# Kernel tuning notes

Measured on AMD Instinct MI355X. Metric: run time of the kernel, lower is better.

Reference implementation:

```python
import jax, jax.numpy as jnp
import numpy as np

H = 4                      # attention heads
N_A, N_P = 20000, 30000    # author / paper node counts
E = 200000                 # edges per edge type
IN, HID, OUT = 256, 256, 128
NEG_SLOPE = 0.2


def setup_inputs() -> dict:
    key = jax.random.key(0)
    ks = jax.random.split(key, 24)

    def w(k, shape, fan_in):
        return jax.random.normal(k, shape, jnp.float32) / np.float32(np.sqrt(fan_in))

    inp = {
        'x_author': jax.random.normal(ks[0], (N_A, IN), jnp.float32),
        'x_paper':  jax.random.normal(ks[1], (N_P, IN), jnp.float32),
        'src_ap': jax.random.randint(ks[2], (E,), 0, N_A, jnp.int32),
        'dst_ap': jax.random.randint(ks[3], (E,), 0, N_P, jnp.int32),
        'src_pa': jax.random.randint(ks[4], (E,), 0, N_P, jnp.int32),
        'dst_pa': jax.random.randint(ks[5], (E,), 0, N_A, jnp.int32),
        'src_pp': jax.random.randint(ks[6], (E,), 0, N_P, jnp.int32),
        'dst_pp': jax.random.randint(ks[7], (E,), 0, N_P, jnp.int32),
        'src_aa': jax.random.randint(ks[8], (E,), 0, N_A, jnp.int32),
        'dst_aa': jax.random.randint(ks[9], (E,), 0, N_A, jnp.int32),
        # layer 1 params
        'W1_a': w(ks[10], (IN, HID), IN), 'b1_a': jnp.zeros((HID,), jnp.float32),
        'W1_p': w(ks[11], (IN, HID), IN), 'b1_p': jnp.zeros((HID,), jnp.float32),
        'att1_src': w(ks[12], (4, H, HID // H), HID // H),
        'att1_dst': w(ks[13], (4, H, HID // H), HID // H),
        'q1': w(ks[14], (HID,), HID),
        'k1_W': w(ks[15], (HID, HID), HID), 'k1_b': jnp.zeros((HID,), jnp.float32),
        # layer 2 params
        'W2_a': w(ks[16], (HID, OUT), HID), 'b2_a': jnp.zeros((OUT,), jnp.float32),
        'W2_p': w(ks[17], (HID, OUT), HID), 'b2_p': jnp.zeros((OUT,), jnp.float32),
        'att2_src': w(ks[18], (4, H, OUT // H), OUT // H),
        'att2_dst': w(ks[19], (4, H, OUT // H), OUT // H),
        'q2': w(ks[20], (OUT,), OUT),
        'k2_W': w(ks[21], (OUT, OUT), OUT), 'k2_b': jnp.zeros((OUT,), jnp.float32),
    }
    return inp


def _han_layer(h, edges, att_src, att_dst, q, kW, kb, sizes):
    """One HANConv layer. h: dict node_type -> [N, H, D]."""
    outs = {nt: [] for nt in h}
    for i, (st, dt, row, col) in enumerate(edges):
        xs, xd = h[st], h[dt]
        nd = sizes[dt]
        # per-edge additive attention logits  [E, H]
        a = jax.nn.leaky_relu((xs * att_src[i]).sum(-1)[row]
                              + (xd * att_dst[i]).sum(-1)[col], NEG_SLOPE)
        # softmax over incoming edges of each dst node (segment softmax)
        amax = jax.ops.segment_max(a, col, num_segments=nd)
        ea = jnp.exp(a - amax[col])
        denom = jax.ops.segment_sum(ea, col, num_segments=nd)
        alpha = ea / (denom[col] + 1e-16)
        # weighted scatter-sum of source features  [Nd, H, D]
        agg = jax.ops.segment_sum(xs[row] * alpha[:, :, None], col, num_segments=nd)
        outs[dt].append(jax.nn.relu(agg.reshape(nd, -1)))
    # semantic (metapath-level) attention: PyG group()
    res = {}
    for nt, lst in outs.items():
        stk = jnp.stack(lst)  # [M, N, F]
        score = (q * jnp.tanh(stk @ kW + kb).mean(axis=1)).sum(-1)  # [M]
        attn = jax.nn.softmax(score, axis=0)
        res[nt] = jnp.einsum('m,mnf->nf', attn, stk)
    return res


def reference(x_author, x_paper, src_ap, dst_ap, src_pa, dst_pa, src_pp, dst_pp,
              src_aa, dst_aa, W1_a, b1_a, W1_p, b1_p, att1_src, att1_dst, q1,
              k1_W, k1_b, W2_a, b2_a, W2_p, b2_p, att2_src, att2_dst, q2,
              k2_W, k2_b):
    sizes = {'author': N_A, 'paper': N_P}
    edges = [('author', 'paper', src_ap, dst_ap),
             ('paper', 'author', src_pa, dst_pa),
             ('paper', 'paper', src_pp, dst_pp),
             ('author', 'author', src_aa, dst_aa)]
    d1 = W1_a.shape[1] // H
    h1 = {'author': (x_author @ W1_a + b1_a).reshape(N_A, H, d1),
          'paper':  (x_paper @ W1_p + b1_p).reshape(N_P, H, d1)}
    x1 = _han_layer(h1, edges, att1_src, att1_dst, q1, k1_W, k1_b, sizes)
    d2 = W2_a.shape[1] // H
    h2 = {'author': (x1['author'] @ W2_a + b2_a).reshape(N_A, H, d2),
          'paper':  (x1['paper'] @ W2_p + b2_p).reshape(N_P, H, d2)}
    x2 = _han_layer(h2, edges, att2_src, att2_dst, q2, k2_W, k2_b, sizes)
    return x2['author']
```

## Files before the change

kernel.cpp:

```cpp
#include <hip/hip_runtime.h>
#include <math.h>


#define NA 20000
#define NP 30000
#define NE 200000
#define D1 256
#define D2 128

typedef __attribute__((ext_vector_type(8))) short short8v;
typedef __attribute__((ext_vector_type(4))) float floatx4;
typedef __attribute__((ext_vector_type(8))) unsigned short ushort8v;
typedef __attribute__((ext_vector_type(4))) unsigned short ushort4v;

static __device__ __forceinline__ float lrelu(float x) { return x >= 0.f ? x : 0.2f * x; }

static __device__ __forceinline__ unsigned short bftrunc(float x) {
    return (unsigned short)(__float_as_uint(x) >> 16);
}
static __device__ __forceinline__ float bf2f(unsigned short b) {
    return __uint_as_float(((unsigned)b) << 16);
}
static __device__ __forceinline__ unsigned short bfrn(float x) {
    unsigned u = __float_as_uint(x);
    return (unsigned short)((u + 0x7FFFu + ((u >> 16) & 1u)) >> 16);
}

typedef __attribute__((address_space(1))) const unsigned int as1_uint;
typedef __attribute__((address_space(3))) unsigned int as3_uint;
static __device__ __forceinline__ void gl_lds16(const void* g, void* l) {
    __builtin_amdgcn_global_load_lds((as1_uint*)g, (as3_uint*)l, 16, 0, 0);
}

static inline int cdiv(int a, int b) { return (a + b - 1) / b; }

struct CsrBatch {
    const int* srcv[4];
    const int* dstv[4];
    int* cnt[4];
    int* csrc[4];
    int* cdst[4];
};

__global__ __launch_bounds__(256) void count_deg_b(CsrBatch c, int n) {
    const int ty = blockIdx.y;
    const int i = blockIdx.x * 256 + threadIdx.x;
    if (i < n) atomicAdd(&c.cnt[ty][c.dstv[ty][i]], 1);
}

__global__ __launch_bounds__(256) void fill_csr_b(CsrBatch c, int n) {
    const int ty = blockIdx.y;
    const int i = blockIdx.x * 256 + threadIdx.x;
    if (i < n) {
        const int d = c.dstv[ty][i];
        const int p = atomicAdd(&c.cnt[ty][d], 1);
        c.csrc[ty][p] = c.srcv[ty][i];
        c.cdst[ty][p] = d;
    }
}

__global__ __launch_bounds__(1024) void exscan4(int* __restrict__ curbase,
                                                int* __restrict__ rpbase) {
    const int off_c[4] = {0, NP, NP + NA, NP + NA + NP};
    const int off_r[4] = {0, NP + 1, NP + NA + 2, NP + NA + NP + 3};
    const int ns[4] = {NP, NA, NP, NA};
    const int b = blockIdx.x;
    int* cur = curbase + off_c[b];
    int* rp = rpbase + off_r[b];
    const int n = ns[b];
    __shared__ int wsum[16];
    __shared__ int carry_s;
    const int t = threadIdx.x, wv = t >> 6, ln = t & 63;
    if (t == 0) carry_s = 0;
    __syncthreads();
    for (int base = 0; base < n; base += 1024) {
        const int i = base + t;
        const int v = (i < n) ? cur[i] : 0;
        int x = v;
#pragma unroll
        for (int off = 1; off < 64; off <<= 1) {
            int y = __shfl_up(x, off);
            if (ln >= off) x += y;
        }
        if (ln == 63) wsum[wv] = x;
        __syncthreads();
        if (wv == 0) {
            int s = (ln < 16) ? wsum[ln] : 0;
#pragma unroll
            for (int off = 1; off < 16; off <<= 1) {
                int y = __shfl_up(s, off);
                if (ln >= off) s += y;
            }
            if (ln < 16) wsum[ln] = s;
        }
        __syncthreads();
        const int woff = (wv == 0) ? 0 : wsum[wv - 1];
        const int c = carry_s;
        const int ex = c + woff + x - v;
        if (i < n) { rp[i] = ex; cur[i] = ex; }
        __syncthreads();
        if (t == 1023) carry_s = c + wsum[15];
        __syncthreads();
    }
    if (t == 0) rp[n] = carry_s;
}

struct PrepBatch {
    const float* W[6];
    unsigned short* img[6];
    int N[6];
    int nsl[6];
};

__global__ __launch_bounds__(256) void w_prep(PrepBatch p) {
    const int m = blockIdx.y;
    const int idx = blockIdx.x * 256 + threadIdx.x;
    if (idx >= p.nsl[m]) return;
    const int N = p.N[m];
    const int slot = idx & 3;
    const int col = (idx >> 2) % N;
    const int rest = (idx >> 2) / N;
    const int part = rest & 1;
    const int kt = rest >> 1;
    const int ks = slot ^ ((col >> 1) & 3);
    unsigned short* dst = p.img[m] + (((size_t)(kt * 2 + part) * N + col) * 32) + slot * 8;
    const float* wsrc = p.W[m] + (size_t)(kt * 32 + ks * 8) * N + col;
    short8v o;
#pragma unroll
    for (int k = 0; k < 8; ++k) {
        const float x = wsrc[(size_t)k * N];
        const unsigned short hb = bftrunc(x);
        o[k] = part ? (short)bftrunc(x - bf2f(hb)) : (short)hb;
    }
    *(short8v*)dst = o;
}

struct XrBatch {
    const float* x[2];
    unsigned short* o[2];
    int n8[2];
};

__global__ __launch_bounds__(256) void xround_b(XrBatch p) {
    const int m = blockIdx.y;
    const int i = blockIdx.x * 256 + threadIdx.x;
    if (i >= p.n8[m]) return;
    const float* xp = p.x[m] + (size_t)i * 8;
    float4 v0 = *(const float4*)xp;
    float4 v1 = *(const float4*)(xp + 4);
    const float xs8[8] = {v0.x, v0.y, v0.z, v0.w, v1.x, v1.y, v1.z, v1.w};
    short8v o;
#pragma unroll
    for (int k = 0; k < 8; ++k) o[k] = (short)bfrn(xs8[k]);
    *(short8v*)&p.o[m][(size_t)i * 8] = o;
}

template <int NT>
struct GemmBatch {
    const unsigned short* A[NT];
    const unsigned short* Wimg[NT];
    const float* bias[NT];
    unsigned short* C[NT];
    int M[NT];
};

template <int BN, bool SCORE, int NT>
__global__ __launch_bounds__(256) void gemm_sw(
    GemmBatch<NT> g, const float* __restrict__ qv, float* __restrict__ score, int K) {
    constexpr int WGN = BN / 64;
    constexpr int WGM = 4 / WGN;
    constexpr int BM = WGM * 64;
    constexpr int ACH = BM * 32 * 2 / 1024;
    constexpr int BCH = 2 * BN * 32 * 2 / 1024;
    constexpr int CPW = (ACH + BCH) / 4;
    const int ty = blockIdx.y;
    const int M = g.M[ty];
    const int bm = blockIdx.x * BM;
    if (bm >= M) return;
    const unsigned short* __restrict__ A = g.A[ty];
    const unsigned short* __restrict__ Wi = g.Wimg[ty];
    const float* __restrict__ bias = g.bias[ty];
    __shared__ __attribute__((aligned(16))) unsigned short As[BM][32];
    __shared__ __attribute__((aligned(16))) unsigned short Bs[2][BN][32];
    const int t = threadIdx.x;
    const int lane = t & 63, wid = t >> 6;
    const int wr = wid / WGN, wc = wid % WGN;
    const int fq = lane >> 4, fr = lane & 15;
    const int asl = (fq ^ ((fr >> 1) & 3)) * 16;
    const int lr = lane >> 2;
    const int lks = (lane & 3) ^ ((lane >> 3) & 3);
    floatx4 acc[4][4];
#pragma unroll
    for (int i = 0; i < 4; ++i)
#pragma unroll
        for (int j = 0; j < 4; ++j) acc[i][j] = {0.f, 0.f, 0.f, 0.f};

    for (int kt = 0; kt < K; kt += 32) {
        const char* wbase = (const char*)Wi + (size_t)(kt >> 5) * (2 * BN * 32 * 2);
#pragma unroll
        for (int ci = 0; ci < CPW; ++ci) {
            const int c = wid * CPW + ci;
            if (c < ACH) {
                const int row = c * 16 + lr;
                const char* srcp = (const char*)(A + (size_t)(bm + row) * K + kt + lks * 8);
                gl_lds16(srcp, (char*)As + c * 1024);
            } else {
                const int bc = c - ACH;
                gl_lds16(wbase + (size_t)bc * 1024 + lane * 16, (char*)Bs + bc * 1024);
            }
        }
        __syncthreads();
        short8v a[4], bh[4], bl[4];
#pragma unroll
        for (int f = 0; f < 4; ++f) {
            const int ar = wr * 64 + f * 16 + fr;
            a[f] = *(const short8v*)((const char*)As + ar * 64 + asl);
            const int bc = wc * 64 + f * 16 + fr;
            bh[f] = *(const short8v*)((const char*)Bs + bc * 64 + asl);
            bl[f] = *(const short8v*)((const char*)Bs + (size_t)BN * 64 + bc * 64 + asl);
        }
#pragma unroll
        for (int i = 0; i < 4; ++i)
#pragma unroll
            for (int j = 0; j < 4; ++j) {
                acc[i][j] = __builtin_amdgcn_mfma_f32_16x16x32_bf16(a[i], bh[j], acc[i][j], 0, 0, 0);
                acc[i][j] = __builtin_amdgcn_mfma_f32_16x16x32_bf16(a[i], bl[j], acc[i][j], 0, 0, 0);
            }
        __syncthreads();
    }
    if constexpr (!SCORE) {
        unsigned short* __restrict__ Cb = g.C[ty];
#pragma unroll
        for (int i = 0; i < 4; ++i) {
            const int gr0 = bm + wr * 64 + i * 16 + fq * 4;
#pragma unroll
            for (int j = 0; j < 4; ++j) {
                const int col = wc * 64 + j * 16 + fr;
                const float b = bias[col];
#pragma unroll
                for (int r = 0; r < 4; ++r) {
                    const int gr = gr0 + r;
                    if (gr < M) Cb[(size_t)gr * BN + col] = bfrn(acc[i][j][r] + b);
                }
            }
        }
    } else {
        __shared__ float red[256];
        float partial = 0.f;
#pragma unroll
        for (int i = 0; i < 4; ++i) {
            const int gr0 = bm + wr * 64 + i * 16 + fq * 4;
#pragma unroll
            for (int j = 0; j < 4; ++j) {
                const int col = wc * 64 + j * 16 + fr;
                const float b = bias[col], q = qv[col];
#pragma unroll
                for (int r = 0; r < 4; ++r) {
                    if (gr0 + r < M) partial += tanhf(acc[i][j][r] + b) * q;
                }
            }
        }
        red[t] = partial;
        __syncthreads();
        for (int s = 128; s > 0; s >>= 1) {
            if (t < s) red[t] += red[t + s];
            __syncthreads();
        }
        if (t == 0) atomicAdd(&score[ty], red[0]);
    }
}

template <int HD, int NSC>
__global__ __launch_bounds__(256) void node_scoresN(
    const unsigned short* __restrict__ hx,
    const float* __restrict__ a0, const float* __restrict__ a1,
    const float* __restrict__ a2, const float* __restrict__ a3,
    float* __restrict__ o0, float* __restrict__ o1,
    float* __restrict__ o2, float* __restrict__ o3, int n) {
    const int idx = blockIdx.x * blockDim.x + threadIdx.x;
    const int node = idx >> 2, hh = idx & 3;
    if (node >= n) return;
    const unsigned short* row = hx + (size_t)node * (4 * HD) + hh * HD;
    float s0 = 0.f, s1 = 0.f, s2 = 0.f, s3 = 0.f;
#pragma unroll
    for (int d = 0; d < HD; d += 4) {
        ushort4v xv = *(const ushort4v*)&row[d];
        const float x0 = bf2f(xv[0]), x1 = bf2f(xv[1]), x2 = bf2f(xv[2]), x3 = bf2f(xv[3]);
        float4 v = *(const float4*)&a0[hh * HD + d];
        s0 += x0 * v.x + x1 * v.y + x2 * v.z + x3 * v.w;
        if constexpr (NSC > 1) {
            v = *(const float4*)&a1[hh * HD + d];
            s1 += x0 * v.x + x1 * v.y + x2 * v.z + x3 * v.w;
        }
        if constexpr (NSC > 2) {
            v = *(const float4*)&a2[hh * HD + d];
            s2 += x0 * v.x + x1 * v.y + x2 * v.z + x3 * v.w;
        }
        if constexpr (NSC > 3) {
            v = *(const float4*)&a3[hh * HD + d];
            s3 += x0 * v.x + x1 * v.y + x2 * v.z + x3 * v.w;
        }
    }
    o0[idx] = s0;
    if constexpr (NSC > 1) o1[idx] = s1;
    if constexpr (NSC > 2) o2[idx] = s2;
    if constexpr (NSC > 3) o3[idx] = s3;
}

template <int NT>
struct ElogBatch {
    const int* csrc[NT];
    const int* cdst[NT];
    const float* ss[NT];
    const float* sd[NT];
    float4* alog[NT];
};

template <int NT>
__global__ __launch_bounds__(256) void edge_logits_b(ElogBatch<NT> a, int n) {
    const int ty = blockIdx.y;
    const int i = blockIdx.x * 256 + threadIdx.x;
    if (i >= n) return;
    const int s = a.csrc[ty][i], d = a.cdst[ty][i];
    const float4 av = *(const float4*)&a.ss[ty][s * 4];
    const float4 bv = *(const float4*)&a.sd[ty][d * 4];
    float4 o = {lrelu(av.x + bv.x), lrelu(av.y + bv.y), lrelu(av.z + bv.z), lrelu(av.w + bv.w)};
    a.alog[ty][i] = o;
}

template <int EPL>
static __device__ __forceinline__ void accum(const unsigned short* p, float ea, float* acc) {
#pragma unroll
    for (int w = 0; w < EPL / 8; ++w) {
        ushort8v x = *(const ushort8v*)(p + w * 8);
#pragma unroll
        for (int k = 0; k < 8; ++k) acc[w * 8 + k] += bf2f(x[k]) * ea;
    }
}

template <int NT>
struct AggBatch {
    const unsigned short* xs[NT];
    const float* alog[NT];
    const int* csrc[NT];
    const int* rowptr[NT];
    unsigned short* out[NT];
    int ndst[NT];
};

template <int D, int NT>
__global__ __launch_bounds__(256) void agg_b(AggBatch<NT> a) {
    constexpr int EPL = D / 16;
    const int ty = blockIdx.y;
    const int gid = blockIdx.x * 16 + (threadIdx.x >> 4);
    if (gid >= a.ndst[ty]) return;
    const int g = threadIdx.x & 15;
    const int h = g >> 2, sub = g & 3;
    const int* __restrict__ rp = a.rowptr[ty];
    const int e0 = rp[gid], e1 = rp[gid + 1];
    const float* __restrict__ lg = a.alog[ty];
    const int* __restrict__ cs = a.csrc[ty];
    const unsigned short* __restrict__ xs = a.xs[ty];
    float mx = -INFINITY;
    for (int e = e0 + sub; e < e1; e += 4)
        mx = fmaxf(mx, lg[(size_t)e * 4 + h]);
    mx = fmaxf(mx, __shfl_xor(mx, 1));
    mx = fmaxf(mx, __shfl_xor(mx, 2));
    float acc[EPL] = {};
    float denom = 0.f;
    int e = e0;
    for (; e + 2 <= e1; e += 2) {
        const int r0 = cs[e], r1 = cs[e + 1];
        const float l0 = lg[(size_t)e * 4 + h];
        const float l1 = lg[(size_t)(e + 1) * 4 + h];
        const float ea0 = __expf(l0 - mx), ea1 = __expf(l1 - mx);
        denom += ea0 + ea1;
        accum<EPL>(xs + (size_t)r0 * D + g * EPL, ea0, acc);
        accum<EPL>(xs + (size_t)r1 * D + g * EPL, ea1, acc);
    }
    if (e < e1) {
        const int r0 = cs[e];
        const float l0 = lg[(size_t)e * 4 + h];
        const float ea0 = __expf(l0 - mx);
        denom += ea0;
        accum<EPL>(xs + (size_t)r0 * D + g * EPL, ea0, acc);
    }
    const float inv = 1.f / (denom + 1e-16f);
    unsigned short* __restrict__ orow = a.out[ty] + (size_t)gid * D + g * EPL;
#pragma unroll
    for (int w = 0; w < EPL / 8; ++w) {
        short8v o;
#pragma unroll
        for (int k = 0; k < 8; ++k)
            o[k] = (short)bfrn(fmaxf(acc[w * 8 + k] * inv, 0.f));
        *(short8v*)&orow[w * 8] = o;
    }
}

struct CombBatch {
    const unsigned short* a[2];
    const unsigned short* b[2];
    unsigned short* o[2];
    int n8[2];
    int slot[2];
    float invN[2];
};

__global__ __launch_bounds__(256) void combine_b(CombBatch c, const float* __restrict__ sc) {
    const int ty = blockIdx.y;
    const int i = blockIdx.x * 256 + threadIdx.x;
    if (i >= c.n8[ty]) return;
    const float s0 = sc[c.slot[ty]] * c.invN[ty];
    const float s1 = sc[c.slot[ty] + 1] * c.invN[ty];
    const float m = fmaxf(s0, s1);
    const float e0 = expf(s0 - m), e1 = expf(s1 - m);
    const float w0 = e0 / (e0 + e1), w1 = e1 / (e0 + e1);
    const size_t o = (size_t)i * 8;
    ushort8v x = *(const ushort8v*)&c.a[ty][o];
    ushort8v y = *(const ushort8v*)&c.b[ty][o];
    short8v r;
#pragma unroll
    for (int k = 0; k < 8; ++k)
        r[k] = (short)bfrn(w0 * bf2f(x[k]) + w1 * bf2f(y[k]));
    *(short8v*)&c.o[ty][o] = r;
}

__global__ __launch_bounds__(256) void combine_out(
    const unsigned short* __restrict__ a, const unsigned short* __restrict__ b,
    float* __restrict__ out, const float* __restrict__ sc, int slot, float invN, int n8) {
    const int i = blockIdx.x * 256 + threadIdx.x;
    if (i >= n8) return;
    const float s0 = sc[slot] * invN, s1 = sc[slot + 1] * invN;
    const float m = fmaxf(s0, s1);
    const float e0 = expf(s0 - m), e1 = expf(s1 - m);
    const float w0 = e0 / (e0 + e1), w1 = e1 / (e0 + e1);
    const size_t o = (size_t)i * 8;
    ushort8v x = *(const ushort8v*)&a[o];
    ushort8v y = *(const ushort8v*)&b[o];
    float rr[8];
#pragma unroll
    for (int k = 0; k < 8; ++k) rr[k] = w0 * bf2f(x[k]) + w1 * bf2f(y[k]);
    float4 r0 = {rr[0], rr[1], rr[2], rr[3]};
    float4 r1 = {rr[4], rr[5], rr[6], rr[7]};
    *(float4*)&out[o] = r0;
    *(float4*)&out[o + 4] = r1;
}

extern "C" void kernel_launch(void* const* d_in, const int* in_sizes, int n_in,
                              void* d_out, int out_size, void* d_ws, size_t ws_size,
                              hipStream_t stream) {
    const float* x_a = (const float*)d_in[0];
    const float* x_p = (const float*)d_in[1];
    const int* src[4] = {(const int*)d_in[2], (const int*)d_in[4], (const int*)d_in[6], (const int*)d_in[8]};
    const int* dst[4] = {(const int*)d_in[3], (const int*)d_in[5], (const int*)d_in[7], (const int*)d_in[9]};
    const float* W1a = (const float*)d_in[10]; const float* b1a = (const float*)d_in[11];
    const float* W1p = (const float*)d_in[12]; const float* b1p = (const float*)d_in[13];
    const float* att1s = (const float*)d_in[14]; const float* att1d = (const float*)d_in[15];
    const float* q1 = (const float*)d_in[16];
    const float* k1W = (const float*)d_in[17]; const float* k1b = (const float*)d_in[18];
    const float* W2a = (const float*)d_in[19]; const float* b2a = (const float*)d_in[20];
    const float* W2p = (const float*)d_in[21]; const float* b2p = (const float*)d_in[22];
    const float* att2s = (const float*)d_in[23]; const float* att2d = (const float*)d_in[24];
    const float* q2 = (const float*)d_in[25];
    const float* k2W = (const float*)d_in[26]; const float* k2b = (const float*)d_in[27];

    const int NAp = NA + 128, NPp = NP + 128;
    char* wp = (char*)d_ws;
    unsigned short* xa_bf = (unsigned short*)wp; wp += (size_t)NAp * D1 * 2;
    unsigned short* xp_bf = (unsigned short*)wp; wp += (size_t)NPp * D1 * 2;
    unsigned short* h1a_bf = (unsigned short*)wp; wp += (size_t)NA * D1 * 2;
    unsigned short* h1p_bf = (unsigned short*)wp; wp += (size_t)NP * D1 * 2;
    unsigned short* a0 = (unsigned short*)wp; wp += (size_t)NPp * D1 * 2;
    unsigned short* a1 = (unsigned short*)wp; wp += (size_t)NAp * D1 * 2;
    unsigned short* a2 = (unsigned short*)wp; wp += (size_t)NPp * D1 * 2;
    unsigned short* a3 = (unsigned short*)wp; wp += (size_t)NAp * D1 * 2;
    float* sv = (float*)wp; wp += (size_t)(16 * NA + 16 * NP) * 4;
    float4* alogb = (float4*)wp; wp += (size_t)4 * NE * 16;
    float* sc = (float*)wp; wp += 16 * 4;
    int* rp_base = (int*)wp; wp += (size_t)(NP + NA + NP + NA + 4) * 4;
    int* cur_base = (int*)wp; wp += (size_t)(NP + NA + NP + NA) * 4;
    int* csrc_base = (int*)wp; wp += (size_t)4 * NE * 4;
    int* cdst_base = (int*)wp; wp += (size_t)4 * NE * 4;
    unsigned short* img_w1a = (unsigned short*)wp; wp += (size_t)8 * 2 * 256 * 32 * 2;
    unsigned short* img_w1p = (unsigned short*)wp; wp += (size_t)8 * 2 * 256 * 32 * 2;
    unsigned short* img_k1w = (unsigned short*)wp; wp += (size_t)8 * 2 * 256 * 32 * 2;
    unsigned short* img_w2a = (unsigned short*)wp; wp += (size_t)8 * 2 * 128 * 32 * 2;
    unsigned short* img_w2p = (unsigned short*)wp; wp += (size_t)8 * 2 * 128 * 32 * 2;
    unsigned short* img_k2w = (unsigned short*)wp; wp += (size_t)4 * 2 * 128 * 32 * 2;
    const size_t need_bytes = (size_t)(wp - (char*)d_ws);
    if (ws_size < need_bytes) return;

    int* rp[4] = {rp_base, rp_base + NP + 1, rp_base + NP + NA + 2, rp_base + NP + NA + NP + 3};
    int* cur[4] = {cur_base, cur_base + NP, cur_base + NP + NA, cur_base + NP + NA + NP};
    int* csrc[4]; int* cdst[4]; float4* alog[4];
    for (int i = 0; i < 4; ++i) {
        csrc[i] = csrc_base + (size_t)i * NE;
        cdst[i] = cdst_base + (size_t)i * NE;
        alog[i] = alogb + (size_t)i * NE;
    }
    float* ss0 = sv;             float* sd0 = ss0 + NA * 4;
    float* ss1 = sd0 + NP * 4;   float* sd1 = ss1 + NP * 4;
    float* ss2 = sd1 + NA * 4;   float* sd2 = ss2 + NP * 4;
    float* ss3 = sd2 + NP * 4;   float* sd3 = ss3 + NA * 4;
    unsigned short* res_p = a0;
    unsigned short* res_a = a1;
    unsigned short* h2a_bf = a2;
    unsigned short* h2p_bf = a2 + (size_t)NA * D2;
    unsigned short* g21 = a3;
    unsigned short* g23 = a3 + (size_t)NAp * D2;
    float* ss21 = sv;             float* sd21 = ss21 + NP * 4;
    float* ss23 = sd21 + NA * 4;  float* sd23 = ss23 + NA * 4;

    hipMemsetAsync(cur_base, 0, (size_t)(NP + NA + NP + NA) * sizeof(int), stream);
    hipMemsetAsync(sc, 0, 16 * sizeof(float), stream);
    PrepBatch pb = {{W1a, W1p, k1W, W2a, W2p, k2W},
                    {img_w1a, img_w1p, img_k1w, img_w2a, img_w2p, img_k2w},
                    {256, 256, 256, 128, 128, 128},
                    {8 * 2 * 256 * 4, 8 * 2 * 256 * 4, 8 * 2 * 256 * 4,
                     8 * 2 * 128 * 4, 8 * 2 * 128 * 4, 4 * 2 * 128 * 4}};
    w_prep<<<dim3(cdiv(8 * 2 * 256 * 4, 256), 6), 256, 0, stream>>>(pb);
    XrBatch xb = {{x_a, x_p}, {xa_bf, xp_bf}, {NA * D1 / 8, NP * D1 / 8}};
    xround_b<<<dim3(cdiv(NP * D1 / 8, 256), 2), 256, 0, stream>>>(xb);

    CsrBatch cb;
    for (int i = 0; i < 4; ++i) {
        cb.srcv[i] = src[i]; cb.dstv[i] = dst[i];
        cb.cnt[i] = cur[i]; cb.csrc[i] = csrc[i]; cb.cdst[i] = cdst[i];
    }
    count_deg_b<<<dim3(cdiv(NE, 256), 4), 256, 0, stream>>>(cb, NE);
    exscan4<<<4, 1024, 0, stream>>>(cur_base, rp_base);
    fill_csr_b<<<dim3(cdiv(NE, 256), 4), 256, 0, stream>>>(cb, NE);

    GemmBatch<2> t1 = {{xa_bf, xp_bf}, {img_w1a, img_w1p}, {b1a, b1p}, {h1a_bf, h1p_bf}, {NA, NP}};
    gemm_sw<256, false, 2><<<dim3(cdiv(NP, 64), 2), 256, 0, stream>>>(t1, nullptr, nullptr, 256);

    node_scoresN<64, 4><<<cdiv(NA * 4, 256), 256, 0, stream>>>(
        h1a_bf, att1s + 0 * 256, att1d + 1 * 256, att1s + 3 * 256, att1d + 3 * 256,
        ss0, sd1, ss3, sd3, NA);
    node_scoresN<64, 4><<<cdiv(NP * 4, 256), 256, 0, stream>>>(
        h1p_bf, att1d + 0 * 256, att1s + 1 * 256, att1s + 2 * 256, att1d + 2 * 256,
        sd0, ss1, ss2, sd2, NP);

    ElogBatch<4> el1 = {{csrc[0], csrc[1], csrc[2], csrc[3]},
                        {cdst[0], cdst[1], cdst[2], cdst[3]},
                        {ss0, ss1, ss2, ss3}, {sd0, sd1, sd2, sd3},
                        {alog[0], alog[1], alog[2], alog[3]}};
    edge_logits_b<4><<<dim3(cdiv(NE, 256), 4), 256, 0, stream>>>(el1, NE);
    AggBatch<4> ab1 = {{h1a_bf, h1p_bf, h1p_bf, h1a_bf},
                       {(const float*)alog[0], (const float*)alog[1], (const float*)alog[2], (const float*)alog[3]},
                       {csrc[0], csrc[1], csrc[2], csrc[3]},
                       {rp[0], rp[1], rp[2], rp[3]},
                       {a0, a1, a2, a3},
                       {NP, NA, NP, NA}};
    agg_b<256, 4><<<dim3(cdiv(NP, 16), 4), 256, 0, stream>>>(ab1);

    GemmBatch<4> s1 = {{a0, a2, a1, a3},
                       {img_k1w, img_k1w, img_k1w, img_k1w},
                       {k1b, k1b, k1b, k1b},
                       {nullptr, nullptr, nullptr, nullptr},
                       {NP, NP, NA, NA}};
    gemm_sw<256, true, 4><<<dim3(cdiv(NP, 64), 4), 256, 0, stream>>>(s1, q1, sc, 256);
    CombBatch c1 = {{a0, a1}, {a2, a3}, {res_p, res_a},
                    {NP * D1 / 8, NA * D1 / 8}, {0, 2}, {1.f / NP, 1.f / NA}};
    combine_b<<<dim3(cdiv(NP * D1 / 8, 256), 2), 256, 0, stream>>>(c1, sc);

    GemmBatch<2> t2 = {{res_a, res_p}, {img_w2a, img_w2p}, {b2a, b2p}, {h2a_bf, h2p_bf}, {NA, NP}};
    gemm_sw<128, false, 2><<<dim3(cdiv(NP, 128), 2), 256, 0, stream>>>(t2, nullptr, nullptr, 256);

    node_scoresN<32, 3><<<cdiv(NA * 4, 256), 256, 0, stream>>>(
        h2a_bf, att2d + 1 * 128, att2s + 3 * 128, att2d + 3 * 128, nullptr,
        sd21, ss23, sd23, nullptr, NA);
    node_scoresN<32, 1><<<cdiv(NP * 4, 256), 256, 0, stream>>>(
        h2p_bf, att2s + 1 * 128, nullptr, nullptr, nullptr,
        ss21, nullptr, nullptr, nullptr, NP);
    ElogBatch<2> el2 = {{csrc[1], csrc[3]}, {cdst[1], cdst[3]},
                        {ss21, ss23}, {sd21, sd23}, {alog[1], alog[3]}};
    edge_logits_b<2><<<dim3(cdiv(NE, 256), 2), 256, 0, stream>>>(el2, NE);
    AggBatch<2> ab2 = {{h2p_bf, h2a_bf},
                       {(const float*)alog[1], (const float*)alog[3]},
                       {csrc[1], csrc[3]}, {rp[1], rp[3]},
                       {g21, g23}, {NA, NA}};
    agg_b<128, 2><<<dim3(cdiv(NA, 16), 2), 256, 0, stream>>>(ab2);

    GemmBatch<2> s2 = {{g21, g23}, {img_k2w, img_k2w}, {k2b, k2b}, {nullptr, nullptr}, {NA, NA}};
    gemm_sw<128, true, 2><<<dim3(cdiv(NA, 128), 2), 256, 0, stream>>>(s2, q2, sc + 4, 128);
    combine_out<<<cdiv(NA * D2 / 8, 256), 256, 0, stream>>>(
        g21, g23, (float*)d_out, sc, 4, 1.f / NA, NA * D2 / 8);
}
```

Baseline: 426.2 us.

## Double-buffer GEMM LDS tiles and drop split-weight MFMA in score GEMMs

The GEMM kernel now double-buffers its A and B shared-memory tiles, so the next K-slice is fetched while the current one feeds the MFMAs, and one barrier per iteration is removed. A new SPLITW template flag lets the score GEMMs skip the second (low-part) weight tile and its extra MFMA, halving their matrix work and weight traffic. The cost is more LDS per block, which may lower occupancy. The score GEMMs also lose the extra precision that the hi/lo weight split gave.

```diff
diff --git a/kernel.cpp b/kernel.cpp
--- a/kernel.cpp
+++ b/kernel.cpp
@@ -164,15 +164,18 @@
     int M[NT];
 };
 
-template <int BN, bool SCORE, int NT>
+template <int BN, bool SCORE, bool SPLITW, int NT>
 __global__ __launch_bounds__(256) void gemm_sw(
     GemmBatch<NT> g, const float* __restrict__ qv, float* __restrict__ score, int K) {
     constexpr int WGN = BN / 64;
     constexpr int WGM = 4 / WGN;
     constexpr int BM = WGM * 64;
+    constexpr int NB = SPLITW ? 2 : 1;
     constexpr int ACH = BM * 32 * 2 / 1024;
-    constexpr int BCH = 2 * BN * 32 * 2 / 1024;
+    constexpr int BCH = NB * BN * 32 * 2 / 1024;
     constexpr int CPW = (ACH + BCH) / 4;
+    constexpr int ASZ = BM * 64;
+    constexpr int BSZ = NB * BN * 64;
     const int ty = blockIdx.y;
     const int M = g.M[ty];
     const int bm = blockIdx.x * BM;
@@ -180,8 +183,9 @@
     const unsigned short* __restrict__ A = g.A[ty];
     const unsigned short* __restrict__ Wi = g.Wimg[ty];
     const float* __restrict__ bias = g.bias[ty];
-    __shared__ __attribute__((aligned(16))) unsigned short As[BM][32];
-    __shared__ __attribute__((aligned(16))) unsigned short Bs[2][BN][32];
+    __shared__ __attribute__((aligned(16))) unsigned short As[2][BM][32];
+    __shared__ __attribute__((aligned(16))) unsigned short Bs[2][NB][BN][32];
+    __shared__ float red[256];
     const int t = threadIdx.x;
     const int lane = t & 63, wid = t >> 6;
     const int wr = wid / WGN, wc = wid % WGN;
@@ -195,38 +199,47 @@
 #pragma unroll
         for (int j = 0; j < 4; ++j) acc[i][j] = {0.f, 0.f, 0.f, 0.f};
 
-    for (int kt = 0; kt < K; kt += 32) {
-        const char* wbase = (const char*)Wi + (size_t)(kt >> 5) * (2 * BN * 32 * 2);
+    const int NK = K >> 5;
+    auto STAGE = [&](int b, int ki) {
+        const char* wbase = (const char*)Wi + (size_t)ki * (2 * BN * 64);
 #pragma unroll
         for (int ci = 0; ci < CPW; ++ci) {
             const int c = wid * CPW + ci;
             if (c < ACH) {
                 const int row = c * 16 + lr;
-                const char* srcp = (const char*)(A + (size_t)(bm + row) * K + kt + lks * 8);
-                gl_lds16(srcp, (char*)As + c * 1024);
+                const char* srcp = (const char*)(A + (size_t)(bm + row) * K + ki * 32 + lks * 8);
+                gl_lds16(srcp, (char*)As + b * ASZ + c * 1024);
             } else {
                 const int bc = c - ACH;
-                gl_lds16(wbase + (size_t)bc * 1024 + lane * 16, (char*)Bs + bc * 1024);
+                gl_lds16(wbase + (size_t)bc * 1024 + lane * 16, (char*)Bs + b * BSZ + bc * 1024);
             }
         }
-        __syncthreads();
+    };
+    STAGE(0, 0);
+    __syncthreads();
+    int cur = 0;
+    for (int ki = 0; ki < NK; ++ki) {
+        if (ki + 1 < NK) STAGE(cur ^ 1, ki + 1);
         short8v a[4], bh[4], bl[4];
 #pragma unroll
         for (int f = 0; f < 4; ++f) {
             const int ar = wr * 64 + f * 16 + fr;
-            a[f] = *(const short8v*)((const char*)As + ar * 64 + asl);
+            a[f] = *(const short8v*)((const char*)As + cur * ASZ + ar * 64 + asl);
             const int bc = wc * 64 + f * 16 + fr;
-            bh[f] = *(const short8v*)((const char*)Bs + bc * 64 + asl);
-            bl[f] = *(const short8v*)((const char*)Bs + (size_t)BN * 64 + bc * 64 + asl);
+            bh[f] = *(const short8v*)((const char*)Bs + cur * BSZ + bc * 64 + asl);
+            if constexpr (SPLITW)
+                bl[f] = *(const short8v*)((const char*)Bs + cur * BSZ + (size_t)BN * 64 + bc * 64 + asl);
         }
 #pragma unroll
         for (int i = 0; i < 4; ++i)
 #pragma unroll
             for (int j = 0; j < 4; ++j) {
                 acc[i][j] = __builtin_amdgcn_mfma_f32_16x16x32_bf16(a[i], bh[j], acc[i][j], 0, 0, 0);
-                acc[i][j] = __builtin_amdgcn_mfma_f32_16x16x32_bf16(a[i], bl[j], acc[i][j], 0, 0, 0);
+                if constexpr (SPLITW)
+                    acc[i][j] = __builtin_amdgcn_mfma_f32_16x16x32_bf16(a[i], bl[j], acc[i][j], 0, 0, 0);
             }
         __syncthreads();
+        cur ^= 1;
     }
     if constexpr (!SCORE) {
         unsigned short* __restrict__ Cb = g.C[ty];
@@ -245,7 +258,6 @@
             }
         }
     } else {
-        __shared__ float red[256];
         float partial = 0.f;
 #pragma unroll
         for (int i = 0; i < 4; ++i) {
@@ -532,7 +544,7 @@
     fill_csr_b<<<dim3(cdiv(NE, 256), 4), 256, 0, stream>>>(cb, NE);
 
     GemmBatch<2> t1 = {{xa_bf, xp_bf}, {img_w1a, img_w1p}, {b1a, b1p}, {h1a_bf, h1p_bf}, {NA, NP}};
-    gemm_sw<256, false, 2><<<dim3(cdiv(NP, 64), 2), 256, 0, stream>>>(t1, nullptr, nullptr, 256);
+    gemm_sw<256, false, true, 2><<<dim3(cdiv(NP, 64), 2), 256, 0, stream>>>(t1, nullptr, nullptr, 256);
 
     node_scoresN<64, 4><<<cdiv(NA * 4, 256), 256, 0, stream>>>(
         h1a_bf, att1s + 0 * 256, att1d + 1 * 256, att1s + 3 * 256, att1d + 3 * 256,
@@ -559,13 +571,13 @@
                        {k1b, k1b, k1b, k1b},
                        {nullptr, nullptr, nullptr, nullptr},
                        {NP, NP, NA, NA}};
-    gemm_sw<256, true, 4><<<dim3(cdiv(NP, 64), 4), 256, 0, stream>>>(s1, q1, sc, 256);
+    gemm_sw<256, true, false, 4><<<dim3(cdiv(NP, 64), 4), 256, 0, stream>>>(s1, q1, sc, 256);
     CombBatch c1 = {{a0, a1}, {a2, a3}, {res_p, res_a},
                     {NP * D1 / 8, NA * D1 / 8}, {0, 2}, {1.f / NP, 1.f / NA}};
     combine_b<<<dim3(cdiv(NP * D1 / 8, 256), 2), 256, 0, stream>>>(c1, sc);
 
     GemmBatch<2> t2 = {{res_a, res_p}, {img_w2a, img_w2p}, {b2a, b2p}, {h2a_bf, h2p_bf}, {NA, NP}};
-    gemm_sw<128, false, 2><<<dim3(cdiv(NP, 128), 2), 256, 0, stream>>>(t2, nullptr, nullptr, 256);
+    gemm_sw<128, false, true, 2><<<dim3(cdiv(NP, 128), 2), 256, 0, stream>>>(t2, nullptr, nullptr, 256);
 
     node_scoresN<32, 3><<<cdiv(NA * 4, 256), 256, 0, stream>>>(
         h2a_bf, att2d + 1 * 128, att2s + 3 * 128, att2d + 3 * 128, nullptr,
@@ -583,7 +595,7 @@
     agg_b<128, 2><<<dim3(cdiv(NA, 16), 2), 256, 0, stream>>>(ab2);
 
     GemmBatch<2> s2 = {{g21, g23}, {img_k2w, img_k2w}, {k2b, k2b}, {nullptr, nullptr}, {NA, NA}};
-    gemm_sw<128, true, 2><<<dim3(cdiv(NA, 128), 2), 256, 0, stream>>>(s2, q2, sc + 4, 128);
+    gemm_sw<128, true, false, 2><<<dim3(cdiv(NA, 128), 2), 256, 0, stream>>>(s2, q2, sc + 4, 128);
     combine_out<<<cdiv(NA * D2 / 8, 256), 256, 0, stream>>>(
         g21, g23, (float*)d_out, sc, 4, 1.f / NA, NA * D2 / 8);
 }
```

Result: faster. 417.0 us (-2.2%).
